# Performance work log

Measured on AMD Instinct MI355X. Metric: run time of the kernel, lower is better.

The kernel has to match this reference:

```python
import jax, jax.numpy as jnp
import numpy as np
from jax import lax

ROT_ANG = 2.0 * np.pi
EPS_FFT = 1e-15
EPS_NORM = 1e-12


def _bilinear_sample(img, px, py):
    # img: [B, C, H, W]; px, py: [n, n] pixel coords. Zero padding outside.
    H, W = img.shape[-2], img.shape[-1]
    x0 = jnp.floor(px)
    y0 = jnp.floor(py)
    wx1 = px - x0
    wy1 = py - y0
    wx0 = 1.0 - wx1
    wy0 = 1.0 - wy1

    def gather(yf, xf, w):
        valid = (yf >= 0) & (yf <= H - 1) & (xf >= 0) & (xf <= W - 1)
        yc = jnp.clip(yf, 0, H - 1).astype(jnp.int32)
        xc = jnp.clip(xf, 0, W - 1).astype(jnp.int32)
        vals = img[:, :, yc, xc]  # [B, C, n, n]
        return vals * (w * valid)[None, None]

    return (gather(y0, x0, wy0 * wx0) + gather(y0, x0 + 1, wy0 * wx1)
            + gather(y0 + 1, x0, wy1 * wx0) + gather(y0 + 1, x0 + 1, wy1 * wx1))


def _radon(img, angles):
    # Parallel-beam Radon: sinogram[b, c, a, s] = line integral along direction
    # (cos a, sin a) at detector offset s (bilinear interp, zero outside image).
    n = img.shape[-1]
    c = (n - 1) / 2.0
    grid = jnp.arange(n, dtype=jnp.float32) - c  # centered coords
    s = grid[:, None]  # detector offset  [n, 1]
    t = grid[None, :]  # along-ray coord  [1, n]

    def one_angle(_, theta):
        ct, st = jnp.cos(theta), jnp.sin(theta)
        px = c + s * ct - t * st  # [n, n]
        py = c + s * st + t * ct
        vals = _bilinear_sample(img, px, py)  # [B, C, n, n]
        return None, vals.sum(-1)  # integrate along ray -> [B, C, n]

    _, sino = lax.scan(one_angle, None, angles)  # [A, B, C, n]
    return jnp.moveaxis(sino, 0, 2)  # [B, C, A, n]


def _forward(bev):
    B = bev.shape[0]
    n_angles = bev.shape[-2]
    angles = jnp.asarray(np.linspace(0.0, ROT_ANG, n_angles).astype(np.float32))
    sinogram = _radon(bev, angles)  # [B, C, A, n]
    # forward_row_fft: 1D FFT along last dim (ortho), magnitude with eps
    f = jnp.fft.fft(sinogram, axis=-1, norm='ortho')
    spec = jnp.sqrt(jnp.real(f) ** 2 + jnp.imag(f) ** 2 + EPS_FFT)
    x = spec.sum(axis=-2).reshape(B, -1)  # sum over angle dim -> [B, C*n]
    # F.normalize(x, dim=-1)
    x = x / jnp.maximum(jnp.linalg.norm(x, axis=-1, keepdims=True), EPS_NORM)
    return x


def setup_inputs() -> dict:
    key = jax.random.key(0)
    bev = jax.random.uniform(key, (1024, 1, 120, 120), dtype=jnp.float32)
    return {"bev": bev}


def reference(bev):
    return _forward(bev)
```

## Files before the change

kernel.cpp:

```cpp
#include <hip/hip_runtime.h>
#include <hip/hip_fp16.h>
#include <math.h>

#define NPIX  120
#define NS    120
#define NK    61
#define HSTR  123
#define HROWS 123
#define CHUNK 8
#define NCHUNK 15
#define NT    1024
#define NGO   488

#if __has_builtin(__builtin_amdgcn_fractf)
#define FRACTF(x) __builtin_amdgcn_fractf(x)
#else
#define FRACTF(x) ((x) - floorf(x))
#endif

__device__ __forceinline__ __half2 lo_h2(uint2 q) { return *reinterpret_cast<__half2*>(&q.x); }
__device__ __forceinline__ __half2 hi_h2(uint2 q) { return *reinterpret_cast<__half2*>(&q.y); }


__global__ void ring_fused(const float* __restrict__ bev,
                           float* __restrict__ out,
                           int B) {
    __shared__ uint2  H[HROWS * HSTR];
    __shared__ float4 schunk[2][CHUNK * NS];
    __shared__ float4 outAcc[NK];
    __shared__ float  invN[4];

    const int tid = threadIdx.x;
    const int b0  = blockIdx.x * 4;
    const int al  = tid >> 7;
    const int sk  = tid & 127;
    const int alg = tid / NK;
    const int kg  = tid - alg * NK;
    if (b0 >= B) return;

    const float* s0 = bev + (size_t)b0 * (NPIX * NPIX);
    const float* s1 = (b0 + 1 < B) ? bev + (size_t)(b0 + 1) * (NPIX * NPIX) : s0;
    const float* s2 = (b0 + 2 < B) ? bev + (size_t)(b0 + 2) * (NPIX * NPIX) : s0;
    const float* s3 = (b0 + 3 < B) ? bev + (size_t)(b0 + 3) * (NPIX * NPIX) : s0;
    for (int i = tid; i < HROWS * HSTR; i += NT) {
        int y = i / HSTR, x = i - y * HSTR;
        float va = 0.f, vb = 0.f, vc = 0.f, vd = 0.f;
        int gx = x - 1, gy = y - 1;
        if (gx >= 0 && gx < NPIX && gy >= 0 && gy < NPIX) {
            int o = gy * NPIX + gx;
            va = s0[o]; vb = s1[o]; vc = s2[o]; vd = s3[o];
        }
        __half2 ab = __floats2half2_rn(va, vb);
        __half2 cd = __floats2half2_rn(vc, vd);
        H[i] = make_uint2(*reinterpret_cast<unsigned*>(&ab),
                          *reinterpret_cast<unsigned*>(&cd));
    }
    __syncthreads();

    const float coef = 2.f * cosf((float)kg * 0.052359877559829887f);
    const float sgn  = (kg & 1) ? -1.f : 1.f;
    const double STEP = 6.283185307179586 / 119.0;
    float acc0 = 0.f, acc1 = 0.f, acc2 = 0.f, acc3 = 0.f;

    for (int ch = 0; ch < NCHUNK; ++ch) {
        float4* buf = schunk[ch & 1];
        if (sk < NS) {
            int a = ch * CHUNK + al;
            float theta = (float)((double)a * STEP);
            float st = sinf(theta), ct = cosf(theta);
            float sf  = (float)sk - 59.5f;
            float Ax  = fmaf(sf, ct, 60.5f);
            float Ay  = fmaf(sf, st, 60.5f);
            float nst = -st;
            const __half2 z2 = __float2half2_rn(0.f);
            float aA = 0.f, aB = 0.f, aC = 0.f, aD = 0.f;
            float tv  = -59.5f;
            for (int tg = 0; tg < 15; ++tg) {
                __half2 sAB0 = z2, sAB1 = z2, sCD0 = z2, sCD1 = z2;
                #pragma unroll
                for (int u = 0; u < 8; ++u) {
                    float px = fmaf(tv, nst, Ax);
                    float py = fmaf(tv, ct,  Ay);
                    float cx = fminf(fmaxf(px, 0.f), 121.5f);
                    float cy = fminf(fmaxf(py, 0.f), 121.5f);
                    int   ix = (int)cx;
                    int   iy = (int)cy;
                    float wx = FRACTF(cx);
                    float wy = FRACTF(cy);
                    int   ai = __mul24(iy, HSTR) + ix;
                    uint2 q00 = H[ai];
                    uint2 q01 = H[ai + 1];
                    uint2 q10 = H[ai + HSTR];
                    uint2 q11 = H[ai + HSTR + 1];
                    __half2 wx2 = __float2half2_rn(wx);
                    __half2 wy2 = __float2half2_rn(wy);
                    __half2 abT = __hfma2(wx2, __hsub2(lo_h2(q01), lo_h2(q00)), lo_h2(q00));
                    __half2 abB = __hfma2(wx2, __hsub2(lo_h2(q11), lo_h2(q10)), lo_h2(q10));
                    __half2 abV = __hfma2(wy2, __hsub2(abB, abT), abT);
                    __half2 cdT = __hfma2(wx2, __hsub2(hi_h2(q01), hi_h2(q00)), hi_h2(q00));
                    __half2 cdB = __hfma2(wx2, __hsub2(hi_h2(q11), hi_h2(q10)), hi_h2(q10));
                    __half2 cdV = __hfma2(wy2, __hsub2(cdB, cdT), cdT);
                    if (u & 1) { sAB1 = __hadd2(sAB1, abV); sCD1 = __hadd2(sCD1, cdV); }
                    else       { sAB0 = __hadd2(sAB0, abV); sCD0 = __hadd2(sCD0, cdV); }
                    tv += 1.f;
                }
                __half2 sAB = __hadd2(sAB0, sAB1);
                __half2 sCD = __hadd2(sCD0, sCD1);
                aA += __low2float(sAB);  aB += __high2float(sAB);
                aC += __low2float(sCD);  aD += __high2float(sCD);
            }
            buf[al * NS + sk] = make_float4(aA, aB, aC, aD);
        }
        __syncthreads();

        if (tid < NGO) {
            const float4* row = buf + alg * NS;
            float u1a = 0.f, u2a = 0.f, u1b = 0.f, u2b = 0.f;
            float u1c = 0.f, u2c = 0.f, u1d = 0.f, u2d = 0.f;
            #pragma unroll 4
            for (int s = 0; s < 60; ++s) {
                float4 lo = row[s];
                float4 hi = row[s + 60];
                float wa = fmaf(sgn, hi.x, lo.x);
                float wb = fmaf(sgn, hi.y, lo.y);
                float wc = fmaf(sgn, hi.z, lo.z);
                float wd = fmaf(sgn, hi.w, lo.w);
                float va = fmaf(coef, u1a, wa - u2a); u2a = u1a; u1a = va;
                float vb = fmaf(coef, u1b, wb - u2b); u2b = u1b; u1b = vb;
                float vc = fmaf(coef, u1c, wc - u2c); u2c = u1c; u1c = vc;
                float vd = fmaf(coef, u1d, wd - u2d); u2d = u1d; u1d = vd;
            }
            float pa = fmaf(u1a, u1a, fmaf(u2a, u2a, -coef * u1a * u2a));
            float pb = fmaf(u1b, u1b, fmaf(u2b, u2b, -coef * u1b * u2b));
            float pc = fmaf(u1c, u1c, fmaf(u2c, u2c, -coef * u1c * u2c));
            float pd = fmaf(u1d, u1d, fmaf(u2d, u2d, -coef * u1d * u2d));
            pa = fmaxf(pa, 0.f); pb = fmaxf(pb, 0.f);
            pc = fmaxf(pc, 0.f); pd = fmaxf(pd, 0.f);
            acc0 += sqrtf(fmaf(pa, (1.f / 120.f), 1e-15f));
            acc1 += sqrtf(fmaf(pb, (1.f / 120.f), 1e-15f));
            acc2 += sqrtf(fmaf(pc, (1.f / 120.f), 1e-15f));
            acc3 += sqrtf(fmaf(pd, (1.f / 120.f), 1e-15f));
        }
    }
    __syncthreads();

    if (tid < NGO) schunk[0][alg * NS + kg] = make_float4(acc0, acc1, acc2, acc3);
    __syncthreads();
    if (tid < NK) {
        float sa = 0.f, sb = 0.f, sc = 0.f, sd = 0.f;
        for (int a2 = 0; a2 < CHUNK; ++a2) {
            float4 v = schunk[0][a2 * NS + tid];
            sa += v.x; sb += v.y; sc += v.z; sd += v.w;
        }
        outAcc[tid] = make_float4(sa, sb, sc, sd);
    }
    __syncthreads();

    if (tid < 4) {
        float ssq = 0.f;
        for (int k = 0; k < NK; ++k) {
            float v = ((const float*)&outAcc[k])[tid];
            float wgt = (k == 0 || k == 60) ? 1.f : 2.f;
            ssq = fmaf(wgt * v, v, ssq);
        }
        invN[tid] = 1.f / fmaxf(sqrtf(ssq), 1e-12f);
    }
    __syncthreads();

    if (tid < 4 * NPIX) {
        int img = tid / NPIX;
        int j   = tid - img * NPIX;
        int k   = (j <= 60) ? j : (NPIX - j);
        int bb  = b0 + img;
        if (bb < B) {
            float v = ((const float*)&outAcc[k])[img] * invN[img];
            out[(size_t)bb * NPIX + j] = v;
        }
    }
}

extern "C" void kernel_launch(void* const* d_in, const int* in_sizes, int n_in,
                              void* d_out, int out_size, void* d_ws, size_t ws_size,
                              hipStream_t stream) {
    const float* bev = (const float*)d_in[0];
    float* out = (float*)d_out;
    int B = in_sizes[0] / (NPIX * NPIX);
    int grid = (B + 3) / 4;
    hipLaunchKernelGGL(ring_fused, dim3(grid), dim3(NT), 0, stream, bev, out, B);
}
```

Measured before the change: 557.2 us.

## Clip ray sampling to image extent and remap detector lanes for wave balance

```diff
diff --git a/kernel.cpp b/kernel.cpp
--- a/kernel.cpp
+++ b/kernel.cpp
@@ -17,6 +17,11 @@
 #else
 #define FRACTF(x) ((x) - floorf(x))
 #endif
+#if __has_builtin(__builtin_amdgcn_rcpf)
+#define RCPF(x) __builtin_amdgcn_rcpf(x)
+#else
+#define RCPF(x) (1.0f / (x))
+#endif
 
 __device__ __forceinline__ __half2 lo_h2(uint2 q) { return *reinterpret_cast<__half2*>(&q.x); }
 __device__ __forceinline__ __half2 hi_h2(uint2 q) { return *reinterpret_cast<__half2*>(&q.y); }
@@ -33,7 +38,8 @@
     const int tid = threadIdx.x;
     const int b0  = blockIdx.x * 4;
     const int al  = tid >> 7;
-    const int sk  = tid & 127;
+    const int skl = tid & 127;
+    const int s_r = (skl < 32) ? skl : ((skl < 64) ? (151 - skl) : (skl - 32));
     const int alg = tid / NK;
     const int kg  = tid - alg * NK;
     if (b0 >= B) return;
@@ -64,19 +70,41 @@
 
     for (int ch = 0; ch < NCHUNK; ++ch) {
         float4* buf = schunk[ch & 1];
-        if (sk < NS) {
+        if (skl < NS) {
             int a = ch * CHUNK + al;
             float theta = (float)((double)a * STEP);
             float st = sinf(theta), ct = cosf(theta);
-            float sf  = (float)sk - 59.5f;
+            float sf  = (float)s_r - 59.5f;
             float Ax  = fmaf(sf, ct, 60.5f);
             float Ay  = fmaf(sf, st, 60.5f);
             float nst = -st;
+
+            float Ax0 = fmaf(-59.5f, nst, Ax);
+            float Ay0 = fmaf(-59.5f, ct,  Ay);
+            float tlo = 0.f, thi = 119.f;
+            if (fabsf(nst) > 1e-5f) {
+                float r  = RCPF(nst);
+                float e1 = (-1.5f - Ax0) * r;
+                float e2 = (123.f - Ax0) * r;
+                tlo = fmaxf(tlo, fminf(e1, e2));
+                thi = fminf(thi, fmaxf(e1, e2));
+            }
+            if (fabsf(ct) > 1e-5f) {
+                float r  = RCPF(ct);
+                float e1 = (-1.5f - Ay0) * r;
+                float e2 = (123.f - Ay0) * r;
+                tlo = fmaxf(tlo, fminf(e1, e2));
+                thi = fminf(thi, fmaxf(e1, e2));
+            }
+            int t0 = (int)fmaxf(tlo, 0.f);
+            int t1 = min(119, (int)fminf(thi, 119.f) + 1);
+            int g0 = t0 >> 3, g1 = t1 >> 3;
+
             const __half2 z2 = __float2half2_rn(0.f);
             float aA = 0.f, aB = 0.f, aC = 0.f, aD = 0.f;
-            float tv  = -59.5f;
-            for (int tg = 0; tg < 15; ++tg) {
+            for (int tg = g0; tg <= g1; ++tg) {
                 __half2 sAB0 = z2, sAB1 = z2, sCD0 = z2, sCD1 = z2;
+                float tv = fmaf(8.f, (float)tg, -59.5f);
                 #pragma unroll
                 for (int u = 0; u < 8; ++u) {
                     float px = fmaf(tv, nst, Ax);
@@ -109,7 +137,7 @@
                 aA += __low2float(sAB);  aB += __high2float(sAB);
                 aC += __low2float(sCD);  aD += __high2float(sCD);
             }
-            buf[al * NS + sk] = make_float4(aA, aB, aC, aD);
+            buf[al * NS + s_r] = make_float4(aA, aB, aC, aD);
         }
         __syncthreads();
 
```

After: 562.2 us. No clear change (+0.9%).
